# Kernel optimization log

Measured on AMD Instinct MI355X. Metric: run time of the kernel, lower is better.

The kernel has to match this reference:

```python
import jax, jax.numpy as jnp
import numpy as np

ATTN_SCALE = 0.12  # attn_args.attn_scale (constant hyperparameter)
EPS = 1e-6         # F.rms_norm eps
GATE_IN = 12       # attn_gate input features (x[..., :12])


def rms_norm(x):
    return x * jax.lax.rsqrt(jnp.mean(x * x, axis=-1, keepdims=True) + EPS)


def rotary(x, cos, sin):
    # x: [B,T,H,D]; cos/sin: [T,D//2]
    x1, x2 = jnp.split(x, 2, axis=-1)
    c = cos[None, :, None, :]
    s = sin[None, :, None, :]
    return jnp.concatenate([x1 * c + x2 * s, -x1 * s + x2 * c], axis=-1)


def setup_inputs() -> dict:
    key = jax.random.key(0)
    ks = jax.random.split(key, 5)
    B, T, D, H, HD = 1, 2048, 1024, 8, 128
    std = 0.5 * D ** -0.5
    x = jax.random.normal(ks[0], (B, T, D), jnp.float32)
    qkvo_w = jax.random.normal(ks[1], (4, D, D), jnp.float32) * std
    gate_w = jax.random.normal(ks[2], (H, GATE_IN), jnp.float32) * 0.02
    ve = jax.random.normal(ks[3], (B, T, H, HD), jnp.float32)
    sa_lambdas = jax.random.uniform(ks[4], (2,), jnp.float32, 0.3, 0.7)
    half = HD // 2
    inv_freq = 1.0 / (10000.0 ** (jnp.arange(half, dtype=jnp.float32) / half))
    ang = jnp.arange(T, dtype=jnp.float32)[:, None] * inv_freq[None, :]
    return dict(x=x, qkvo_w=qkvo_w, gate_w=gate_w, ve=ve,
                sa_lambdas=sa_lambdas, cos=jnp.cos(ang), sin=jnp.sin(ang))


def reference(x, qkvo_w, gate_w, ve, sa_lambdas, cos, sin):
    B, T, D = x.shape
    H = gate_w.shape[0]
    HD = D // H
    # fused QKV projection: rows of qkvo_w[:3] are [q; k; v]
    w_qkv = qkvo_w[:3].reshape(3 * D, D)           # [3D, D]
    qkv = jnp.einsum('btd,ed->bte', x, w_qkv)      # [B,T,3D]
    qkv = qkv.reshape(B, T, 3, H, HD)
    q, k, v = qkv[:, :, 0], qkv[:, :, 1], qkv[:, :, 2]
    # RMSNorm + RoPE on q, k
    q = rotary(rms_norm(q), cos, sin)
    k = rotary(rms_norm(k), cos, sin)
    # value-residual mixing
    v = sa_lambdas[0] * v + sa_lambdas[1] * ve
    # causal SDPA with custom scale
    scores = jnp.einsum('bqhd,bkhd->bhqk', q, k) * ATTN_SCALE
    causal = jnp.tril(jnp.ones((T, T), dtype=bool))
    scores = jnp.where(causal[None, None], scores, jnp.finfo(scores.dtype).min)
    p = jax.nn.softmax(scores, axis=-1)
    y = jnp.einsum('bhqk,bkhd->bqhd', p, v)        # [B,T,H,HD]
    # per-head sigmoid gate from the first 12 channels of x
    gate = jax.nn.sigmoid(jnp.einsum('bti,hi->bth', x[..., :GATE_IN], gate_w))
    y = y * gate[..., None]
    # output projection (qkvo_w[3]): F.linear -> y @ W_o^T
    out = jnp.einsum('bti,oi->bto', y.reshape(B, T, H * HD), qkvo_w[3])
    return out
```

## Files before the change

### kernel.cpp

```cpp
#include <hip/hip_runtime.h>
#include <stdint.h>

typedef unsigned short u16;
typedef unsigned int u32;

typedef __bf16 bfx8 __attribute__((ext_vector_type(8)));
typedef float fx4 __attribute__((ext_vector_type(4)));
typedef float fx16 __attribute__((ext_vector_type(16)));
typedef u16 u16x4 __attribute__((ext_vector_type(4)));
typedef u16 u16x8 __attribute__((ext_vector_type(8)));

#define GAS __attribute__((address_space(1)))
#define LAS __attribute__((address_space(3)))

__device__ __forceinline__ void gload16(const void* g, void* l) {
  __builtin_amdgcn_global_load_lds((GAS void*)g, (LAS void*)l, 16, 0, 0);
}

__device__ __forceinline__ u16 f2bf(float f) {
  union { float f; u32 u; } v; v.f = f;
  u32 r = v.u + 0x7fffu + ((v.u >> 16) & 1u);
  return (u16)(r >> 16);
}
__device__ __forceinline__ float bf2f(u16 u) {
  union { u32 u; float f; } v; v.u = ((u32)u) << 16;
  return v.f;
}

__device__ __forceinline__ int segF(int qb) { return (qb * qb + 2 * qb + (qb & 1)) >> 2; }

__global__ __launch_bounds__(256) void k_cvt(const float* __restrict__ src, u16* __restrict__ dst, int n) {
  int i = (blockIdx.x * 256 + threadIdx.x) * 8;
  if (i >= n) return;
  const float4* s = (const float4*)(src + i);
  float4 a = s[0], b = s[1];
  u16x8 o;
  o[0] = f2bf(a.x); o[1] = f2bf(a.y); o[2] = f2bf(a.z); o[3] = f2bf(a.w);
  o[4] = f2bf(b.x); o[5] = f2bf(b.y); o[6] = f2bf(b.z); o[7] = f2bf(b.w);
  *(u16x8*)(dst + i) = o;
}

__global__ __launch_bounds__(256) void k_gemm_out(const u16* __restrict__ A, const u16* __restrict__ B,
                                                  float* __restrict__ C, int M, int N, int K) {
  __shared__ char sm[16384];
  const int tid = threadIdx.x;
  const int l = tid & 63, w = tid >> 6;
  const int li = l & 15, lg = l >> 4;
  const int bid = (blockIdx.x & 7) * 64 + (blockIdx.x >> 3);
  const int nbm = M >> 6;
  const int bm = bid % nbm, bn = bid / nbm;

  const u16* gsrc[4];
#pragma unroll
  for (int i = 0; i < 4; ++i) {
    int b = i * 4096 + tid * 16;
    int row, ch;
    const u16* mat;
    if (b < 8192) { row = b >> 7; mat = A + (size_t)(bm * 64 + row) * K; }
    else          { int bb = b - 8192; row = bb >> 7; mat = B + (size_t)(bn * 64 + row) * K; }
    ch = ((b >> 4) & 7) ^ (row & 7);
    gsrc[i] = mat + ch * 8;
  }

  fx4 acc[4];
#pragma unroll
  for (int jj = 0; jj < 4; ++jj)
#pragma unroll
    for (int r = 0; r < 4; ++r) acc[jj][r] = 0.f;

  for (int k0 = 0; k0 < K; k0 += 64) {
    __syncthreads();
#pragma unroll
    for (int i = 0; i < 4; ++i) gload16(gsrc[i] + k0, sm + i * 4096 + w * 1024);
    __syncthreads();
#pragma unroll
    for (int kk = 0; kk < 2; ++kk) {
      int rowa = w * 16 + li;
      bfx8 af = *(const bfx8*)(sm + rowa * 128 + (((kk * 4 + lg)) ^ (rowa & 7)) * 16);
#pragma unroll
      for (int nf = 0; nf < 4; ++nf) {
        int rowb = nf * 16 + li;
        bfx8 bfr = *(const bfx8*)(sm + 8192 + rowb * 128 + ((kk * 4 + lg) ^ (rowb & 7)) * 16);
        acc[nf] = __builtin_amdgcn_mfma_f32_16x16x32_bf16(af, bfr, acc[nf], 0, 0, 0);
      }
    }
  }
#pragma unroll
  for (int nf = 0; nf < 4; ++nf)
#pragma unroll
    for (int r = 0; r < 4; ++r) {
      int row = bm * 64 + w * 16 + lg * 4 + r;
      int col = bn * 64 + nf * 16 + li;
      C[(size_t)row * N + col] = acc[nf][r];
    }
}

__global__ __launch_bounds__(256) void k_gemm_qkv(const u16* __restrict__ A, const u16* __restrict__ B,
                                                  u16* __restrict__ qb2, u16* __restrict__ kt2,
                                                  u16* __restrict__ vt2,
                                                  const float* __restrict__ ve, const float* __restrict__ lam,
                                                  const float* __restrict__ cosp, const float* __restrict__ sinp) {
  __shared__ char sm[24576];
  const int tid = threadIdx.x;
  const int l = tid & 63, w = tid >> 6;
  const int li = l & 15, lg = l >> 4;
  const int bid = (blockIdx.x & 7) * 96 + (blockIdx.x >> 3);
  const int bm = bid & 31, bn = bid >> 5;
  const int K = 1024;

  const u16* gsrc[6];
#pragma unroll
  for (int i = 0; i < 6; ++i) {
    int b = i * 4096 + tid * 16;
    int row, ch;
    const u16* mat;
    if (b < 8192) { row = b >> 7; mat = A + (size_t)(bm * 64 + row) * K; }
    else          { int bb = b - 8192; row = bb >> 7; mat = B + (size_t)(bn * 128 + row) * K; }
    ch = ((b >> 4) & 7) ^ (row & 7);
    gsrc[i] = mat + ch * 8;
  }

  fx4 acc[8];
#pragma unroll
  for (int jj = 0; jj < 8; ++jj)
#pragma unroll
    for (int r = 0; r < 4; ++r) acc[jj][r] = 0.f;

  for (int k0 = 0; k0 < K; k0 += 64) {
    __syncthreads();
#pragma unroll
    for (int i = 0; i < 6; ++i) gload16(gsrc[i] + k0, sm + i * 4096 + w * 1024);
    __syncthreads();
#pragma unroll
    for (int kk = 0; kk < 2; ++kk) {
      int rowa = w * 16 + li;
      bfx8 af = *(const bfx8*)(sm + rowa * 128 + ((kk * 4 + lg) ^ (rowa & 7)) * 16);
#pragma unroll
      for (int nf = 0; nf < 8; ++nf) {
        int rowb = nf * 16 + li;
        bfx8 bfr = *(const bfx8*)(sm + 8192 + rowb * 128 + ((kk * 4 + lg) ^ (rowb & 7)) * 16);
        acc[nf] = __builtin_amdgcn_mfma_f32_16x16x32_bf16(af, bfr, acc[nf], 0, 0, 0);
      }
    }
  }

  const int s = bn >> 3, h = bn & 7;
  if (s < 2) {
#pragma unroll
    for (int r = 0; r < 4; ++r) {
      int t = bm * 64 + w * 16 + lg * 4 + r;
      float ss = 0.f;
#pragma unroll
      for (int nf = 0; nf < 8; ++nf) ss += acc[nf][r] * acc[nf][r];
      ss += __shfl_xor(ss, 1); ss += __shfl_xor(ss, 2);
      ss += __shfl_xor(ss, 4); ss += __shfl_xor(ss, 8);
      float rn = rsqrtf(ss * (1.f / 128.f) + 1e-6f);
#pragma unroll
      for (int nf = 0; nf < 4; ++nf) {
        int dp = nf * 16 + li;
        float c = cosp[(size_t)t * 64 + dp];
        float sn = sinp[(size_t)t * 64 + dp];
        float x1 = acc[nf][r] * rn, x2 = acc[nf + 4][r] * rn;
        u16 o1 = f2bf(x1 * c + x2 * sn);
        u16 o2 = f2bf(-x1 * sn + x2 * c);
        if (s == 0) {
          u16* qp = qb2 + (size_t)t * 1024 + h * 128;
          qp[dp] = o1;
          qp[dp + 64] = o2;
        } else {
          u16* kp = kt2 + (size_t)h * 262144 + (size_t)(t >> 5) * 4096 + (t & 31) * 128;
          int dq = dp + 64;
          kp[(((dp >> 3) ^ (t & 7)) << 3) | (dp & 7)] = o1;
          kp[(((dq >> 3) ^ (t & 7)) << 3) | (dq & 7)] = o2;
        }
      }
    }
  } else {
    const float l0 = lam[0], l1 = lam[1];
    int tb = bm * 64 + w * 16 + lg * 4;
    u16* vbase = vt2 + (size_t)h * 262144 + (size_t)(tb >> 5) * 4096 + ((tb & 31) >> 3) * 1024 + (tb & 7);
#pragma unroll
    for (int nf = 0; nf < 8; ++nf) {
      int d = nf * 16 + li;
      u16x4 o;
#pragma unroll
      for (int r = 0; r < 4; ++r)
        o[r] = f2bf(l0 * acc[nf][r] + l1 * ve[(size_t)(tb + r) * 1024 + h * 128 + d]);
      *(u16x4*)(vbase + d * 8) = o;
    }
  }
}

__global__ __launch_bounds__(256) void k_attn2(const u16* __restrict__ qb2, const u16* __restrict__ kt2,
                                               const u16* __restrict__ vt2,
                                               u16* __restrict__ part, float* __restrict__ ml) {
  __shared__ char sm[32768];
  const int bid = (blockIdx.x & 7) * 72 + (blockIdx.x >> 3);
  const int h = bid / 72;
  const int r72 = bid % 72;
  int qb = 15;
  while (segF(qb) > r72) --qb;
  const int s = r72 - segF(qb);
  const int q0 = qb * 128;
  const int seg0 = s * 256;
  const int seg_len = min(256, (qb + 1) * 128 - seg0);
  const int nkt = seg_len >> 5;

  const int tid = threadIdx.x;
  const int l = tid & 63, w = tid >> 6;
  const int li = l & 31, hi = l >> 5;
  const int qrow = q0 + w * 32 + li;
  const int wqmax = q0 + w * 32 + 31;
  const int wqmin = q0 + w * 32;

  bfx8 Q[8];
  {
    const u16* qp = qb2 + (size_t)qrow * 1024 + h * 128 + hi * 8;
#pragma unroll
    for (int c = 0; c < 8; ++c) Q[c] = *(const bfx8*)(qp + c * 16);
  }

  const u16* ktile = kt2 + (size_t)h * 262144 + (size_t)(seg0 >> 5) * 4096;
  const u16* vtile = vt2 + (size_t)h * 262144 + (size_t)(seg0 >> 5) * 4096;

  auto STAGE = [&](int kt, int buf) {
    char* dst = sm + buf * 16384;
    const u16* ks = ktile + (size_t)kt * 4096;
    const u16* vs = vtile + (size_t)kt * 4096;
#pragma unroll
    for (int i = 0; i < 2; ++i) {
      int j = w * 2 + i;
      gload16(ks + j * 512 + l * 8, dst + j * 1024);
      gload16(vs + j * 512 + l * 8, dst + 8192 + j * 1024);
    }
  };

  fx16 Y[4];
#pragma unroll
  for (int d = 0; d < 4; ++d)
#pragma unroll
    for (int r = 0; r < 16; ++r) Y[d][r] = 0.f;
  float m_run = -1e30f, l_run = 0.f;

  STAGE(0, 0);
  __syncthreads();
  int cur = 0;

  for (int kt = 0; kt < nkt; ++kt) {
    if (kt + 1 < nkt) STAGE(kt + 1, cur ^ 1);
    const int k0 = seg0 + kt * 32;
    if (k0 <= wqmax) {
      const char* kb = sm + cur * 16384;
      const char* vb = kb + 8192;
      fx16 S;
#pragma unroll
      for (int r = 0; r < 16; ++r) S[r] = 0.f;
#pragma unroll
      for (int c = 0; c < 8; ++c) {
        int ch = (c * 2 + hi) ^ (li & 7);
        bfx8 kf = *(const bfx8*)(kb + li * 256 + ch * 16);
        S = __builtin_amdgcn_mfma_f32_32x32x16_bf16(kf, Q[c], S, 0, 0, 0);
      }
      const bool nomask = (k0 + 31 <= wqmin);
      float p[16];
      float mt = -1e30f;
#pragma unroll
      for (int r = 0; r < 16; ++r) {
        int kk = (r & 3) + 8 * (r >> 2) + 4 * hi;
        float sv = (nomask || (k0 + kk <= qrow)) ? S[r] * 0.12f : -1e30f;
        p[r] = sv;
        mt = fmaxf(mt, sv);
      }
      mt = fmaxf(mt, __shfl_xor(mt, 32));
      float mnew = fmaxf(m_run, mt);
      float alpha = __expf(m_run - mnew);
      float ssum = 0.f;
#pragma unroll
      for (int r = 0; r < 16; ++r) { float e = __expf(p[r] - mnew); p[r] = e; ssum += e; }
      ssum += __shfl_xor(ssum, 32);
      l_run = l_run * alpha + ssum;
      m_run = mnew;
#pragma unroll
      for (int d = 0; d < 4; ++d)
#pragma unroll
        for (int r = 0; r < 16; ++r) Y[d][r] *= alpha;
      u32 pk[8], pks[8];
#pragma unroll
      for (int i = 0; i < 8; ++i) pk[i] = (u32)f2bf(p[2 * i]) | ((u32)f2bf(p[2 * i + 1]) << 16);
#pragma unroll
      for (int i = 0; i < 8; ++i) pks[i] = (u32)__shfl_xor((int)pk[i], 32);
      union { u32 u[4]; bfx8 v; } P0, P1;
      if (hi == 0) {
        P0.u[0] = pk[0];  P0.u[1] = pk[1];  P0.u[2] = pks[0]; P0.u[3] = pks[1];
        P1.u[0] = pk[4];  P1.u[1] = pk[5];  P1.u[2] = pks[4]; P1.u[3] = pks[5];
      } else {
        P0.u[0] = pks[2]; P0.u[1] = pks[3]; P0.u[2] = pk[2];  P0.u[3] = pk[3];
        P1.u[0] = pks[6]; P1.u[1] = pks[7]; P1.u[2] = pk[6];  P1.u[3] = pk[7];
      }
#pragma unroll
      for (int db = 0; db < 4; ++db) {
        int dd = db * 32 + li;
        bfx8 v0 = *(const bfx8*)(vb + hi * 2048 + dd * 16);
        bfx8 v1 = *(const bfx8*)(vb + (2 + hi) * 2048 + dd * 16);
        Y[db] = __builtin_amdgcn_mfma_f32_32x32x16_bf16(v0, P0.v, Y[db], 0, 0, 0);
        Y[db] = __builtin_amdgcn_mfma_f32_32x32x16_bf16(v1, P1.v, Y[db], 0, 0, 0);
      }
    }
    __syncthreads();
    cur ^= 1;
  }

  if (hi == 0) {
    ml[(size_t)bid * 256 + (w * 32 + li) * 2 + 0] = m_run;
    ml[(size_t)bid * 256 + (w * 32 + li) * 2 + 1] = l_run;
  }
  float* Yl = (float*)(sm + w * 8192);
  u16* pdst = part + (size_t)bid * 16384;
#pragma unroll
  for (int P = 0; P < 2; ++P) {
    asm volatile("" ::: "memory");
#pragma unroll
    for (int dh = 0; dh < 2; ++dh) {
      int db = P * 2 + dh;
#pragma unroll
      for (int r = 0; r < 16; ++r) {
        int dloc = dh * 32 + (r & 3) + 8 * (r >> 2) + 4 * hi;
        Yl[li * 64 + (dloc ^ ((li & 7) << 2))] = Y[db][r];
      }
    }
    asm volatile("" ::: "memory");
    int rr = l >> 1, c0 = (l & 1) * 32, sx = (rr & 7) << 2;
#pragma unroll
    for (int j = 0; j < 8; ++j) {
      float4 v = *(const float4*)(Yl + rr * 64 + ((c0 + j * 4) ^ sx));
      u16x4 o;
      o[0] = f2bf(v.x); o[1] = f2bf(v.y); o[2] = f2bf(v.z); o[3] = f2bf(v.w);
      *(u16x4*)(pdst + (w * 32 + rr) * 128 + P * 64 + c0 + j * 4) = o;
    }
  }
}

__global__ __launch_bounds__(256) void k_comb(const u16* __restrict__ part, const float* __restrict__ ml,
                                              const float* __restrict__ x, const float* __restrict__ gw,
                                              u16* __restrict__ y) {
  const int b = blockIdx.x;
  const int h = b >> 4, qb = b & 15;
  const int nseg = (qb + 2) >> 1;
  const int slot0 = h * 72 + segF(qb);
  const int t = threadIdx.x;
  const int r = t >> 1, hf = (t & 1) * 64;
  const int q = qb * 128 + r;

  float ms[8], ls[8];
  float M = -1e30f;
#pragma unroll
  for (int s = 0; s < 8; ++s) {
    if (s < nseg) {
      ms[s] = ml[(size_t)(slot0 + s) * 256 + r * 2 + 0];
      ls[s] = ml[(size_t)(slot0 + s) * 256 + r * 2 + 1];
      M = fmaxf(M, ms[s]);
    }
  }
  float wt[8];
  float L = 0.f;
#pragma unroll
  for (int s = 0; s < 8; ++s) {
    if (s < nseg) { wt[s] = __expf(ms[s] - M); L += wt[s] * ls[s]; }
  }
  float accv[64];
#pragma unroll
  for (int j = 0; j < 64; ++j) accv[j] = 0.f;
#pragma unroll
  for (int s = 0; s < 8; ++s) {
    if (s < nseg) {
      const u16x8* P = (const u16x8*)(part + (size_t)(slot0 + s) * 16384 + r * 128 + hf);
      float ws_ = wt[s];
#pragma unroll
      for (int j = 0; j < 8; ++j) {
        u16x8 v = P[j];
#pragma unroll
        for (int e = 0; e < 8; ++e) accv[j * 8 + e] += ws_ * bf2f(v[e]);
      }
    }
  }
  float dot = 0.f;
#pragma unroll
  for (int i = 0; i < 12; ++i) dot += x[(size_t)q * 1024 + i] * gw[h * 12 + i];
  float gt_ = 1.f / (1.f + __expf(-dot));
  float sc = gt_ / L;
  u16* yp = y + (size_t)q * 1024 + h * 128 + hf;
#pragma unroll
  for (int j = 0; j < 8; ++j) {
    u16x8 o;
#pragma unroll
    for (int e = 0; e < 8; ++e) o[e] = f2bf(accv[j * 8 + e] * sc);
    *(u16x8*)(yp + j * 8) = o;
  }
}

extern "C" void kernel_launch(void* const* d_in, const int* in_sizes, int n_in,
                              void* d_out, int out_size, void* d_ws, size_t ws_size,
                              hipStream_t stream) {
  const float* x = (const float*)d_in[0];
  const float* qkvo_w = (const float*)d_in[1];
  const float* gate_w = (const float*)d_in[2];
  const float* ve = (const float*)d_in[3];
  const float* lam = (const float*)d_in[4];
  const float* cosp = (const float*)d_in[5];
  const float* sinp = (const float*)d_in[6];
  float* out = (float*)d_out;

  u16* wb  = (u16*)d_ws;
  u16* xb  = wb + 4u * 1024 * 1024;
  u16* qb2 = xb + 2u * 1024 * 1024;
  u16* kt2 = qb2 + 2u * 1024 * 1024;
  u16* vt2 = kt2 + 2u * 1024 * 1024;
  u16* y   = vt2 + 2u * 1024 * 1024;
  u16* part = y + 2u * 1024 * 1024;
  float* ml = (float*)(part + (size_t)576 * 16384);

  k_cvt<<<dim3(2048), dim3(256), 0, stream>>>(qkvo_w, wb, 4 * 1024 * 1024);
  k_cvt<<<dim3(1024), dim3(256), 0, stream>>>(x, xb, 2 * 1024 * 1024);
  k_gemm_qkv<<<dim3(32 * 24), dim3(256), 0, stream>>>(xb, wb, qb2, kt2, vt2, ve, lam, cosp, sinp);
  k_attn2<<<dim3(576), dim3(256), 0, stream>>>(qb2, kt2, vt2, part, ml);
  k_comb<<<dim3(128), dim3(256), 0, stream>>>(part, ml, x, gate_w, y);
  k_gemm_out<<<dim3(32 * 16), dim3(256), 0, stream>>>(y, wb + 3u * 1024 * 1024, out, 2048, 1024, 1024);
}
```

Baseline: 100.6 us.

## Double the attention key tile from 32 to 64 keys per iteration

The attention kernel now processes 64 keys per loop iteration: it stages two 32-key K/V tiles per buffer (64 KB of shared memory), computes two score blocks, and does a single online-softmax rescale per iteration. This halves the number of barriers, max/sum shuffles and accumulator rescales per segment. In exchange, shared memory use and register pressure rise, which may lower occupancy, and the causal diagonal tile now wastes more masked work. Segment lengths must be multiples of 64 for correctness, and the 128-row granularity appears to guarantee that.

After: 109.6 us. +8.9%, slower.

```diff
diff --git a/kernel.cpp b/kernel.cpp
--- a/kernel.cpp
+++ b/kernel.cpp
@@ -194,7 +194,7 @@
 __global__ __launch_bounds__(256) void k_attn2(const u16* __restrict__ qb2, const u16* __restrict__ kt2,
                                                const u16* __restrict__ vt2,
                                                u16* __restrict__ part, float* __restrict__ ml) {
-  __shared__ char sm[32768];
+  __shared__ char sm[65536];
   const int bid = (blockIdx.x & 7) * 72 + (blockIdx.x >> 3);
   const int h = bid / 72;
   const int r72 = bid % 72;
@@ -204,7 +204,7 @@
   const int q0 = qb * 128;
   const int seg0 = s * 256;
   const int seg_len = min(256, (qb + 1) * 128 - seg0);
-  const int nkt = seg_len >> 5;
+  const int nkt = seg_len >> 6;
 
   const int tid = threadIdx.x;
   const int l = tid & 63, w = tid >> 6;
@@ -224,14 +224,14 @@
   const u16* vtile = vt2 + (size_t)h * 262144 + (size_t)(seg0 >> 5) * 4096;
 
   auto STAGE = [&](int kt, int buf) {
-    char* dst = sm + buf * 16384;
-    const u16* ks = ktile + (size_t)kt * 4096;
-    const u16* vs = vtile + (size_t)kt * 4096;
-#pragma unroll
-    for (int i = 0; i < 2; ++i) {
-      int j = w * 2 + i;
+    char* dst = sm + buf * 32768;
+    const u16* ks = ktile + (size_t)kt * 8192;
+    const u16* vs = vtile + (size_t)kt * 8192;
+#pragma unroll
+    for (int i = 0; i < 4; ++i) {
+      int j = w * 4 + i;
       gload16(ks + j * 512 + l * 8, dst + j * 1024);
-      gload16(vs + j * 512 + l * 8, dst + 8192 + j * 1024);
+      gload16(vs + j * 512 + l * 8, dst + 16384 + j * 1024);
     }
   };
 
@@ -248,35 +248,42 @@
 
   for (int kt = 0; kt < nkt; ++kt) {
     if (kt + 1 < nkt) STAGE(kt + 1, cur ^ 1);
-    const int k0 = seg0 + kt * 32;
+    const int k0 = seg0 + kt * 64;
     if (k0 <= wqmax) {
-      const char* kb = sm + cur * 16384;
-      const char* vb = kb + 8192;
-      fx16 S;
-#pragma unroll
-      for (int r = 0; r < 16; ++r) S[r] = 0.f;
+      const char* kb = sm + cur * 32768;
+      const char* vb = kb + 16384;
+      fx16 S0, S1;
+#pragma unroll
+      for (int r = 0; r < 16; ++r) { S0[r] = 0.f; S1[r] = 0.f; }
 #pragma unroll
       for (int c = 0; c < 8; ++c) {
         int ch = (c * 2 + hi) ^ (li & 7);
-        bfx8 kf = *(const bfx8*)(kb + li * 256 + ch * 16);
-        S = __builtin_amdgcn_mfma_f32_32x32x16_bf16(kf, Q[c], S, 0, 0, 0);
-      }
-      const bool nomask = (k0 + 31 <= wqmin);
-      float p[16];
+        bfx8 kf0 = *(const bfx8*)(kb + li * 256 + ch * 16);
+        bfx8 kf1 = *(const bfx8*)(kb + 8192 + li * 256 + ch * 16);
+        S0 = __builtin_amdgcn_mfma_f32_32x32x16_bf16(kf0, Q[c], S0, 0, 0, 0);
+        S1 = __builtin_amdgcn_mfma_f32_32x32x16_bf16(kf1, Q[c], S1, 0, 0, 0);
+      }
+      const bool nomask = (k0 + 63 <= wqmin);
+      float p0[16], p1[16];
       float mt = -1e30f;
 #pragma unroll
       for (int r = 0; r < 16; ++r) {
         int kk = (r & 3) + 8 * (r >> 2) + 4 * hi;
-        float sv = (nomask || (k0 + kk <= qrow)) ? S[r] * 0.12f : -1e30f;
-        p[r] = sv;
-        mt = fmaxf(mt, sv);
+        float sa = (nomask || (k0 + kk <= qrow)) ? S0[r] * 0.12f : -1e30f;
+        float sb = (nomask || (k0 + 32 + kk <= qrow)) ? S1[r] * 0.12f : -1e30f;
+        p0[r] = sa; p1[r] = sb;
+        mt = fmaxf(mt, fmaxf(sa, sb));
       }
       mt = fmaxf(mt, __shfl_xor(mt, 32));
       float mnew = fmaxf(m_run, mt);
       float alpha = __expf(m_run - mnew);
       float ssum = 0.f;
 #pragma unroll
-      for (int r = 0; r < 16; ++r) { float e = __expf(p[r] - mnew); p[r] = e; ssum += e; }
+      for (int r = 0; r < 16; ++r) {
+        float e0 = __expf(p0[r] - mnew);
+        float e1 = __expf(p1[r] - mnew);
+        p0[r] = e0; p1[r] = e1; ssum += e0 + e1;
+      }
       ssum += __shfl_xor(ssum, 32);
       l_run = l_run * alpha + ssum;
       m_run = mnew;
@@ -284,26 +291,31 @@
       for (int d = 0; d < 4; ++d)
 #pragma unroll
         for (int r = 0; r < 16; ++r) Y[d][r] *= alpha;
-      u32 pk[8], pks[8];
-#pragma unroll
-      for (int i = 0; i < 8; ++i) pk[i] = (u32)f2bf(p[2 * i]) | ((u32)f2bf(p[2 * i + 1]) << 16);
-#pragma unroll
-      for (int i = 0; i < 8; ++i) pks[i] = (u32)__shfl_xor((int)pk[i], 32);
-      union { u32 u[4]; bfx8 v; } P0, P1;
-      if (hi == 0) {
-        P0.u[0] = pk[0];  P0.u[1] = pk[1];  P0.u[2] = pks[0]; P0.u[3] = pks[1];
-        P1.u[0] = pk[4];  P1.u[1] = pk[5];  P1.u[2] = pks[4]; P1.u[3] = pks[5];
-      } else {
-        P0.u[0] = pks[2]; P0.u[1] = pks[3]; P0.u[2] = pk[2];  P0.u[3] = pk[3];
-        P1.u[0] = pks[6]; P1.u[1] = pks[7]; P1.u[2] = pk[6];  P1.u[3] = pk[7];
-      }
-#pragma unroll
-      for (int db = 0; db < 4; ++db) {
-        int dd = db * 32 + li;
-        bfx8 v0 = *(const bfx8*)(vb + hi * 2048 + dd * 16);
-        bfx8 v1 = *(const bfx8*)(vb + (2 + hi) * 2048 + dd * 16);
-        Y[db] = __builtin_amdgcn_mfma_f32_32x32x16_bf16(v0, P0.v, Y[db], 0, 0, 0);
-        Y[db] = __builtin_amdgcn_mfma_f32_32x32x16_bf16(v1, P1.v, Y[db], 0, 0, 0);
+#pragma unroll
+      for (int kbt = 0; kbt < 2; ++kbt) {
+        const float* pp = kbt ? p1 : p0;
+        u32 pk[8], pks[8];
+#pragma unroll
+        for (int i = 0; i < 8; ++i) pk[i] = (u32)f2bf(pp[2 * i]) | ((u32)f2bf(pp[2 * i + 1]) << 16);
+#pragma unroll
+        for (int i = 0; i < 8; ++i) pks[i] = (u32)__shfl_xor((int)pk[i], 32);
+        union { u32 u[4]; bfx8 v; } P0, P1;
+        if (hi == 0) {
+          P0.u[0] = pk[0];  P0.u[1] = pk[1];  P0.u[2] = pks[0]; P0.u[3] = pks[1];
+          P1.u[0] = pk[4];  P1.u[1] = pk[5];  P1.u[2] = pks[4]; P1.u[3] = pks[5];
+        } else {
+          P0.u[0] = pks[2]; P0.u[1] = pks[3]; P0.u[2] = pk[2];  P0.u[3] = pk[3];
+          P1.u[0] = pks[6]; P1.u[1] = pks[7]; P1.u[2] = pk[6];  P1.u[3] = pk[7];
+        }
+        const char* vimg = vb + kbt * 8192;
+#pragma unroll
+        for (int db = 0; db < 4; ++db) {
+          int dd = db * 32 + li;
+          bfx8 v0 = *(const bfx8*)(vimg + hi * 2048 + dd * 16);
+          bfx8 v1 = *(const bfx8*)(vimg + (2 + hi) * 2048 + dd * 16);
+          Y[db] = __builtin_amdgcn_mfma_f32_32x32x16_bf16(v0, P0.v, Y[db], 0, 0, 0);
+          Y[db] = __builtin_amdgcn_mfma_f32_32x32x16_bf16(v1, P1.v, Y[db], 0, 0, 0);
+        }
       }
     }
     __syncthreads();
```

## Replace online-softmax running max with fixed exponent offset from RMS-norm bound

Applied to the files above, without the earlier changes.

After RMSNorm, q and k each have norm sqrt(128), so their dot product is at most 128 and the scaled score is at most 15.36. The attention kernel therefore subtracts a constant 16 before exponentiating instead of tracking a running max. This removes the per-tile max reduction and cross-lane shuffle, the alpha rescale of the 64 output accumulators, and storing m. The combine kernel then just sums the partial l values and partial outputs with no exp reweighting. The risk is reduced dynamic range: very negative scores sit near exp(-31), but that stays well inside float and bf16 range.

Result: faster. 97.75 us (-2.9%).

```diff
diff --git a/kernel.cpp b/kernel.cpp
--- a/kernel.cpp
+++ b/kernel.cpp
@@ -240,7 +240,7 @@
   for (int d = 0; d < 4; ++d)
 #pragma unroll
     for (int r = 0; r < 16; ++r) Y[d][r] = 0.f;
-  float m_run = -1e30f, l_run = 0.f;
+  float l_run = 0.f;
 
   STAGE(0, 0);
   __syncthreads();
@@ -263,27 +263,23 @@
       }
       const bool nomask = (k0 + 31 <= wqmin);
       float p[16];
-      float mt = -1e30f;
-#pragma unroll
-      for (int r = 0; r < 16; ++r) {
-        int kk = (r & 3) + 8 * (r >> 2) + 4 * hi;
-        float sv = (nomask || (k0 + kk <= qrow)) ? S[r] * 0.12f : -1e30f;
-        p[r] = sv;
-        mt = fmaxf(mt, sv);
-      }
-      mt = fmaxf(mt, __shfl_xor(mt, 32));
-      float mnew = fmaxf(m_run, mt);
-      float alpha = __expf(m_run - mnew);
       float ssum = 0.f;
-#pragma unroll
-      for (int r = 0; r < 16; ++r) { float e = __expf(p[r] - mnew); p[r] = e; ssum += e; }
+      if (nomask) {
+#pragma unroll
+        for (int r = 0; r < 16; ++r) {
+          float e = __expf(fmaf(S[r], 0.12f, -16.f));
+          p[r] = e; ssum += e;
+        }
+      } else {
+#pragma unroll
+        for (int r = 0; r < 16; ++r) {
+          int kk = (r & 3) + 8 * (r >> 2) + 4 * hi;
+          float e = (k0 + kk <= qrow) ? __expf(fmaf(S[r], 0.12f, -16.f)) : 0.f;
+          p[r] = e; ssum += e;
+        }
+      }
       ssum += __shfl_xor(ssum, 32);
-      l_run = l_run * alpha + ssum;
-      m_run = mnew;
-#pragma unroll
-      for (int d = 0; d < 4; ++d)
-#pragma unroll
-        for (int r = 0; r < 16; ++r) Y[d][r] *= alpha;
+      l_run += ssum;
       u32 pk[8], pks[8];
 #pragma unroll
       for (int i = 0; i < 8; ++i) pk[i] = (u32)f2bf(p[2 * i]) | ((u32)f2bf(p[2 * i + 1]) << 16);
@@ -310,10 +306,7 @@
     cur ^= 1;
   }
 
-  if (hi == 0) {
-    ml[(size_t)bid * 256 + (w * 32 + li) * 2 + 0] = m_run;
-    ml[(size_t)bid * 256 + (w * 32 + li) * 2 + 1] = l_run;
-  }
+  if (hi == 0) ml[(size_t)bid * 128 + w * 32 + li] = l_run;
   float* Yl = (float*)(sm + w * 8192);
   u16* pdst = part + (size_t)bid * 16384;
 #pragma unroll
@@ -351,22 +344,11 @@
   const int r = t >> 1, hf = (t & 1) * 64;
   const int q = qb * 128 + r;
 
-  float ms[8], ls[8];
-  float M = -1e30f;
-#pragma unroll
-  for (int s = 0; s < 8; ++s) {
-    if (s < nseg) {
-      ms[s] = ml[(size_t)(slot0 + s) * 256 + r * 2 + 0];
-      ls[s] = ml[(size_t)(slot0 + s) * 256 + r * 2 + 1];
-      M = fmaxf(M, ms[s]);
-    }
-  }
-  float wt[8];
   float L = 0.f;
 #pragma unroll
-  for (int s = 0; s < 8; ++s) {
-    if (s < nseg) { wt[s] = __expf(ms[s] - M); L += wt[s] * ls[s]; }
-  }
+  for (int s = 0; s < 8; ++s)
+    if (s < nseg) L += ml[(size_t)(slot0 + s) * 128 + r];
+
   float accv[64];
 #pragma unroll
   for (int j = 0; j < 64; ++j) accv[j] = 0.f;
@@ -374,12 +356,11 @@
   for (int s = 0; s < 8; ++s) {
     if (s < nseg) {
       const u16x8* P = (const u16x8*)(part + (size_t)(slot0 + s) * 16384 + r * 128 + hf);
-      float ws_ = wt[s];
 #pragma unroll
       for (int j = 0; j < 8; ++j) {
         u16x8 v = P[j];
 #pragma unroll
-        for (int e = 0; e < 8; ++e) accv[j * 8 + e] += ws_ * bf2f(v[e]);
+        for (int e = 0; e < 8; ++e) accv[j * 8 + e] += bf2f(v[e]);
       }
     }
   }
```
